# Optimization experiments

Measured on AMD Instinct MI355X. Metric: run time of the kernel, lower is better.

The kernel has to match this reference:

```python
import jax, jax.numpy as jnp
import numpy as np

B, L, H, E = 2, 2048, 16, 64
S, D = L, E


def setup_inputs() -> dict:
    key = jax.random.key(0)
    kq, kk, kv = jax.random.split(key, 3)
    queries = jax.random.normal(kq, (B, L, H, E), dtype=jnp.float32)
    keys = jax.random.normal(kk, (B, S, H, E), dtype=jnp.float32)
    values = jax.random.normal(kv, (B, S, H, D), dtype=jnp.float32)
    return {"queries": queries, "keys": keys, "values": values}


def reference(queries, keys, values):
    # FullAttention forward: mask_flag=True, attn_mask=None -> causal mask,
    # scale=None -> 1/sqrt(E), dropout in eval mode (identity).
    Bq, Lq, Hq, Eq = queries.shape
    Sq = values.shape[1]
    scale = 1.0 / jnp.sqrt(jnp.asarray(Eq, dtype=queries.dtype))
    # [B,H,L,S] score matrix, same as torch.einsum('blhe,bshe->bhls', q, k)
    scores = jnp.einsum('blhe,bshe->bhls', queries, keys)
    # TriangularCausalMask: triu(ones, diagonal=1) -> True above diagonal = masked
    causal = jnp.triu(jnp.ones((Lq, Sq), dtype=bool), k=1)
    scores = jnp.where(causal[None, None, :, :], -jnp.inf, scores)
    A = jax.nn.softmax(scale * scores, axis=-1)
    V = jnp.einsum('bhls,bshd->blhd', A, values)
    return V
```

## Files before the change

### kernel.cpp

```cpp
#include <hip/hip_runtime.h>
#include <hip/hip_bf16.h>


#define B_DIM 2
#define L_DIM 2048
#define H_DIM 16
#define E_DIM 64
#define NEG_INF (-1e30f)
#define CAP   16.0f

typedef __attribute__((ext_vector_type(8))) short short8;
typedef __attribute__((ext_vector_type(4))) float ffrag;

static __device__ __forceinline__ short f2bf(float x) {
    __hip_bfloat16 h = __float2bfloat16(x);
    return *reinterpret_cast<short*>(&h);
}
static __device__ __forceinline__ unsigned pk2(float lo, float hi) {
    __hip_bfloat162 h = __float22bfloat162_rn(make_float2(lo, hi));
    return *reinterpret_cast<unsigned*>(&h);
}

__global__ __launch_bounds__(256, 4)
void attn_fused(const float* __restrict__ Q, const float* __restrict__ K,
                const float* __restrict__ V, float* __restrict__ O) {
    const int lid = blockIdx.x;
    const int x   = lid & 7;
    const int c   = (lid >> 3) & 31;
    const int k4  = lid >> 8;
    const int bh  = x * 4 + k4;
    const int b   = bh >> 4;
    const int h   = bh & 15;
    int strip;
    switch (k4) {
        case 0:  strip = c;              break;
        case 1:  strip = 31 - c;         break;
        case 2:  strip = c ^ 16;         break;
        default: strip = 31 - (c ^ 16);  break;
    }
    const int q0 = strip * 64;

    const int tid  = threadIdx.x;
    const int wave = tid >> 6;
    const int lane = tid & 63;
    const int n16  = lane & 15;
    const int quad = lane >> 4;

    __shared__ short Kt[4096];
    __shared__ short Vt[4096];
    __shared__ short Pq[4096];

    const float sc = 0.125f * 1.44269504088896340736f;
    const int gq = q0 + wave * 16 + n16;

    short8 qf[2];
    {
        const float4* pq = (const float4*)(Q + (((size_t)b * L_DIM + gq) * H_DIM + h) * E_DIM);
#pragma unroll
        for (int kt = 0; kt < 2; ++kt) {
            float4 x0 = pq[kt * 8 + quad * 2];
            float4 x1 = pq[kt * 8 + quad * 2 + 1];
            short8 f;
            f[0] = f2bf(x0.x * sc); f[1] = f2bf(x0.y * sc);
            f[2] = f2bf(x0.z * sc); f[3] = f2bf(x0.w * sc);
            f[4] = f2bf(x1.x * sc); f[5] = f2bf(x1.y * sc);
            f[6] = f2bf(x1.z * sc); f[7] = f2bf(x1.w * sc);
            qf[kt] = f;
        }
    }

    const int rr  = tid >> 2;
    const int c2  = tid & 3;
    const int kOff0 = rr * 64 + (((2 * c2)     ^ (rr & 7)) * 8);
    const int kOff1 = rr * 64 + (((2 * c2 + 1) ^ (rr & 7)) * 8);
    const int kp2 = (tid & 31) * 2;
    const int c8  = (tid >> 5) * 8;

    float4 kr[4], va[2], vb2[2];

    auto load_tile = [&](int kt0) {
        const float4* kg = (const float4*)(K + (((size_t)b * L_DIM + kt0 + rr) * H_DIM + h) * E_DIM + c2 * 16);
        kr[0] = kg[0]; kr[1] = kg[1]; kr[2] = kg[2]; kr[3] = kg[3];
        const float* vp = V + (((size_t)b * L_DIM + kt0 + kp2) * H_DIM + h) * E_DIM + c8;
        const float4* vga = (const float4*)vp;
        const float4* vgb = (const float4*)(vp + H_DIM * E_DIM);
        va[0]  = vga[0]; va[1]  = vga[1];
        vb2[0] = vgb[0]; vb2[1] = vgb[1];
    };
    auto store_tile = [&]() {
        short8 w0, w1;
        w0[0] = f2bf(kr[0].x); w0[1] = f2bf(kr[0].y); w0[2] = f2bf(kr[0].z); w0[3] = f2bf(kr[0].w);
        w0[4] = f2bf(kr[1].x); w0[5] = f2bf(kr[1].y); w0[6] = f2bf(kr[1].z); w0[7] = f2bf(kr[1].w);
        w1[0] = f2bf(kr[2].x); w1[1] = f2bf(kr[2].y); w1[2] = f2bf(kr[2].z); w1[3] = f2bf(kr[2].w);
        w1[4] = f2bf(kr[3].x); w1[5] = f2bf(kr[3].y); w1[6] = f2bf(kr[3].z); w1[7] = f2bf(kr[3].w);
        *(short8*)&Kt[kOff0] = w0;
        *(short8*)&Kt[kOff1] = w1;
        const float* a0 = (const float*)va;
        const float* b0 = (const float*)vb2;
#pragma unroll
        for (int i = 0; i < 8; ++i)
            *(unsigned*)&Vt[(c8 + i) * 64 + (((kp2 >> 3) ^ i) * 8) + (kp2 & 7)] = pk2(a0[i], b0[i]);
    };

    ffrag Oa[4];
#pragma unroll
    for (int nt = 0; nt < 4; ++nt) Oa[nt] = ffrag{0.f, 0.f, 0.f, 0.f};
    float l = 0.f;

    const int sw  = n16 & 7;
    const int fo0 = (quad ^ sw) * 8;
    const int fo1 = fo0 ^ 32;
    short* pbase = &Pq[wave * 1024 + n16 * 64];

    load_tile(0);

    for (int kt0 = 0; kt0 <= q0; kt0 += 64) {
        __syncthreads();
        store_tile();
        __syncthreads();
        if (kt0 + 64 <= q0) load_tile(kt0 + 64);

        ffrag S[4];
#pragma unroll
        for (int mt = 0; mt < 4; ++mt) {
            const int rb = (mt * 16 + n16) * 64;
            short8 a0 = *(const short8*)&Kt[rb + fo0];
            short8 a1 = *(const short8*)&Kt[rb + fo1];
            ffrag z = ffrag{0.f, 0.f, 0.f, 0.f};
            z = __builtin_amdgcn_mfma_f32_16x16x32_bf16(a0, qf[0], z, 0, 0, 0);
            S[mt] = __builtin_amdgcn_mfma_f32_16x16x32_bf16(a1, qf[1], z, 0, 0, 0);
        }

        const bool domask = (kt0 == q0);
        float ps = 0.f;
#pragma unroll
        for (int mt = 0; mt < 4; ++mt) {
            float pv[4];
#pragma unroll
            for (int r = 0; r < 4; ++r) {
                float sv = S[mt][r];
                if (domask && (mt * 16 + quad * 4 + r > wave * 16 + n16)) sv = NEG_INF;
                pv[r] = exp2f(sv - CAP);
                ps += pv[r];
            }
            uint2 w;
            w.x = pk2(pv[0], pv[1]);
            w.y = pk2(pv[2], pv[3]);
            *(uint2*)&pbase[(((2 * mt + (quad >> 1)) ^ sw) * 8) + (quad & 1) * 4] = w;
        }
        ps += __shfl_xor(ps, 16);
        ps += __shfl_xor(ps, 32);
        l += ps;

        short8 pa0 = *(const short8*)&pbase[fo0];
        short8 pa1 = *(const short8*)&pbase[fo1];

#pragma unroll
        for (int nt = 0; nt < 4; ++nt) {
            const int rb = (nt * 16 + n16) * 64;
            short8 b0 = *(const short8*)&Vt[rb + fo0];
            short8 b1 = *(const short8*)&Vt[rb + fo1];
            Oa[nt] = __builtin_amdgcn_mfma_f32_16x16x32_bf16(pa0, b0, Oa[nt], 0, 0, 0);
            Oa[nt] = __builtin_amdgcn_mfma_f32_16x16x32_bf16(pa1, b1, Oa[nt], 0, 0, 0);
        }
    }

#pragma unroll
    for (int r = 0; r < 4; ++r) {
        float li  = __shfl(l, quad * 4 + r);
        float inv = 1.0f / li;
        const int row = q0 + wave * 16 + quad * 4 + r;
        float* op = O + (((size_t)b * L_DIM + row) * H_DIM + h) * E_DIM;
#pragma unroll
        for (int nt = 0; nt < 4; ++nt) op[nt * 16 + n16] = Oa[nt][r] * inv;
    }
}

extern "C" void kernel_launch(void* const* d_in, const int* in_sizes, int n_in,
                              void* d_out, int out_size, void* d_ws, size_t ws_size,
                              hipStream_t stream) {
    const float* Q = (const float*)d_in[0];
    const float* K = (const float*)d_in[1];
    const float* V = (const float*)d_in[2];
    float* O = (float*)d_out;
    attn_fused<<<dim3(1024), 256, 0, stream>>>(Q, K, V, O);
}
```

Baseline: 139.4 us.

## Split KV tiles across two wave groups per block and merge partial outputs

Result: slower. 285.1 us (+104.6%).

```diff
diff --git a/kernel.cpp b/kernel.cpp
--- a/kernel.cpp
+++ b/kernel.cpp
@@ -21,7 +21,7 @@
     return *reinterpret_cast<unsigned*>(&h);
 }
 
-__global__ __launch_bounds__(256, 4)
+__global__ __launch_bounds__(512, 6)
 void attn_fused(const float* __restrict__ Q, const float* __restrict__ K,
                 const float* __restrict__ V, float* __restrict__ O) {
     const int lid = blockIdx.x;
@@ -38,20 +38,25 @@
         case 2:  strip = c ^ 16;         break;
         default: strip = 31 - (c ^ 16);  break;
     }
-    const int q0 = strip * 64;
-
-    const int tid  = threadIdx.x;
-    const int wave = tid >> 6;
-    const int lane = tid & 63;
-    const int n16  = lane & 15;
-    const int quad = lane >> 4;
-
-    __shared__ short Kt[4096];
-    __shared__ short Vt[4096];
-    __shared__ short Pq[4096];
+    const int q0     = strip * 64;
+    const int ntiles = strip + 1;
+    const int T      = (ntiles + 1) >> 1;
+
+    const int tid   = threadIdx.x;
+    const int wave  = tid >> 6;
+    const int grp   = tid >> 8;
+    const int qwave = wave & 3;
+    const int lane  = tid & 63;
+    const int n16   = lane & 15;
+    const int quad  = lane >> 4;
+
+    __shared__ alignas(16) short KV[4][4096];
+    __shared__ alignas(16) short Pq[8192];
+    short* Kt = KV[grp * 2 + 0];
+    short* Vt = KV[grp * 2 + 1];
 
     const float sc = 0.125f * 1.44269504088896340736f;
-    const int gq = q0 + wave * 16 + n16;
+    const int gq = q0 + qwave * 16 + n16;
 
     short8 qf[2];
     {
@@ -69,12 +74,13 @@
         }
     }
 
-    const int rr  = tid >> 2;
-    const int c2  = tid & 3;
+    const int gtid = tid & 255;
+    const int rr  = gtid >> 2;
+    const int c2  = gtid & 3;
     const int kOff0 = rr * 64 + (((2 * c2)     ^ (rr & 7)) * 8);
     const int kOff1 = rr * 64 + (((2 * c2 + 1) ^ (rr & 7)) * 8);
-    const int kp2 = (tid & 31) * 2;
-    const int c8  = (tid >> 5) * 8;
+    const int kp2 = (gtid & 31) * 2;
+    const int c8  = ((gtid >> 5) & 7) * 8;
 
     float4 kr[4], va[2], vb2[2];
 
@@ -112,67 +118,92 @@
     const int fo1 = fo0 ^ 32;
     short* pbase = &Pq[wave * 1024 + n16 * 64];
 
-    load_tile(0);
-
-    for (int kt0 = 0; kt0 <= q0; kt0 += 64) {
+    if (grp == 0 || ntiles > 1) load_tile(grp << 6);
+
+    for (int t = 0; t < T; ++t) {
+        const int it    = 2 * t + grp;
+        const bool valid = (it < ntiles);
         __syncthreads();
-        store_tile();
+        if (valid) store_tile();
         __syncthreads();
-        if (kt0 + 64 <= q0) load_tile(kt0 + 64);
-
-        ffrag S[4];
-#pragma unroll
-        for (int mt = 0; mt < 4; ++mt) {
-            const int rb = (mt * 16 + n16) * 64;
-            short8 a0 = *(const short8*)&Kt[rb + fo0];
-            short8 a1 = *(const short8*)&Kt[rb + fo1];
-            ffrag z = ffrag{0.f, 0.f, 0.f, 0.f};
-            z = __builtin_amdgcn_mfma_f32_16x16x32_bf16(a0, qf[0], z, 0, 0, 0);
-            S[mt] = __builtin_amdgcn_mfma_f32_16x16x32_bf16(a1, qf[1], z, 0, 0, 0);
+        if (it + 2 < ntiles) load_tile((it + 2) << 6);
+
+        if (valid) {
+            ffrag S[4];
+            __builtin_amdgcn_s_setprio(1);
+#pragma unroll
+            for (int mt = 0; mt < 4; ++mt) {
+                const int rb = (mt * 16 + n16) * 64;
+                short8 a0 = *(const short8*)&Kt[rb + fo0];
+                short8 a1 = *(const short8*)&Kt[rb + fo1];
+                ffrag z = ffrag{0.f, 0.f, 0.f, 0.f};
+                z = __builtin_amdgcn_mfma_f32_16x16x32_bf16(a0, qf[0], z, 0, 0, 0);
+                S[mt] = __builtin_amdgcn_mfma_f32_16x16x32_bf16(a1, qf[1], z, 0, 0, 0);
+            }
+            __builtin_amdgcn_s_setprio(0);
+
+            const bool domask = (it == ntiles - 1);
+            float ps = 0.f;
+#pragma unroll
+            for (int mt = 0; mt < 4; ++mt) {
+                float pv[4];
+#pragma unroll
+                for (int r = 0; r < 4; ++r) {
+                    float sv = S[mt][r];
+                    if (domask && (mt * 16 + quad * 4 + r > qwave * 16 + n16)) sv = NEG_INF;
+                    pv[r] = exp2f(sv - CAP);
+                    ps += pv[r];
+                }
+                uint2 w;
+                w.x = pk2(pv[0], pv[1]);
+                w.y = pk2(pv[2], pv[3]);
+                *(uint2*)&pbase[(((2 * mt + (quad >> 1)) ^ sw) * 8) + (quad & 1) * 4] = w;
+            }
+            ps += __shfl_xor(ps, 16);
+            ps += __shfl_xor(ps, 32);
+            l += ps;
+
+            short8 pa0 = *(const short8*)&pbase[fo0];
+            short8 pa1 = *(const short8*)&pbase[fo1];
+
+            __builtin_amdgcn_s_setprio(1);
+#pragma unroll
+            for (int nt = 0; nt < 4; ++nt) {
+                const int rb = (nt * 16 + n16) * 64;
+                short8 b0 = *(const short8*)&Vt[rb + fo0];
+                short8 b1 = *(const short8*)&Vt[rb + fo1];
+                Oa[nt] = __builtin_amdgcn_mfma_f32_16x16x32_bf16(pa0, b0, Oa[nt], 0, 0, 0);
+                Oa[nt] = __builtin_amdgcn_mfma_f32_16x16x32_bf16(pa1, b1, Oa[nt], 0, 0, 0);
+            }
+            __builtin_amdgcn_s_setprio(0);
         }
-
-        const bool domask = (kt0 == q0);
-        float ps = 0.f;
-#pragma unroll
-        for (int mt = 0; mt < 4; ++mt) {
-            float pv[4];
-#pragma unroll
-            for (int r = 0; r < 4; ++r) {
-                float sv = S[mt][r];
-                if (domask && (mt * 16 + quad * 4 + r > wave * 16 + n16)) sv = NEG_INF;
-                pv[r] = exp2f(sv - CAP);
-                ps += pv[r];
-            }
-            uint2 w;
-            w.x = pk2(pv[0], pv[1]);
-            w.y = pk2(pv[2], pv[3]);
-            *(uint2*)&pbase[(((2 * mt + (quad >> 1)) ^ sw) * 8) + (quad & 1) * 4] = w;
+    }
+
+    __syncthreads();
+    float* fO = (float*)&KV[0][0];
+    float* fL = (float*)&KV[2][0];
+    if (grp == 1) {
+        ffrag* dst = (ffrag*)(fO + ((qwave * 64 + lane) << 4));
+#pragma unroll
+        for (int nt = 0; nt < 4; ++nt) dst[nt] = Oa[nt];
+        fL[qwave * 64 + lane] = l;
+    }
+    __syncthreads();
+    if (grp == 0) {
+        const ffrag* src = (const ffrag*)(fO + ((qwave * 64 + lane) << 4));
+#pragma unroll
+        for (int nt = 0; nt < 4; ++nt) Oa[nt] += src[nt];
+        l += fL[qwave * 64 + lane];
+
+#pragma unroll
+        for (int r = 0; r < 4; ++r) {
+            float li  = __shfl(l, quad * 4 + r);
+            float inv = 1.0f / li;
+            const int row = q0 + qwave * 16 + quad * 4 + r;
+            float* op = O + (((size_t)b * L_DIM + row) * H_DIM + h) * E_DIM;
+#pragma unroll
+            for (int nt = 0; nt < 4; ++nt) op[nt * 16 + n16] = Oa[nt][r] * inv;
         }
-        ps += __shfl_xor(ps, 16);
-        ps += __shfl_xor(ps, 32);
-        l += ps;
-
-        short8 pa0 = *(const short8*)&pbase[fo0];
-        short8 pa1 = *(const short8*)&pbase[fo1];
-
-#pragma unroll
-        for (int nt = 0; nt < 4; ++nt) {
-            const int rb = (nt * 16 + n16) * 64;
-            short8 b0 = *(const short8*)&Vt[rb + fo0];
-            short8 b1 = *(const short8*)&Vt[rb + fo1];
-            Oa[nt] = __builtin_amdgcn_mfma_f32_16x16x32_bf16(pa0, b0, Oa[nt], 0, 0, 0);
-            Oa[nt] = __builtin_amdgcn_mfma_f32_16x16x32_bf16(pa1, b1, Oa[nt], 0, 0, 0);
-        }
-    }
-
-#pragma unroll
-    for (int r = 0; r < 4; ++r) {
-        float li  = __shfl(l, quad * 4 + r);
-        float inv = 1.0f / li;
-        const int row = q0 + wave * 16 + quad * 4 + r;
-        float* op = O + (((size_t)b * L_DIM + row) * H_DIM + h) * E_DIM;
-#pragma unroll
-        for (int nt = 0; nt < 4; ++nt) op[nt * 16 + n16] = Oa[nt][r] * inv;
     }
 }
 
@@ -183,5 +214,5 @@
     const float* K = (const float*)d_in[1];
     const float* V = (const float*)d_in[2];
     float* O = (float*)d_out;
-    attn_fused<<<dim3(1024), 256, 0, stream>>>(Q, K, V, O);
-}
+    attn_fused<<<dim3(1024), 512, 0, stream>>>(Q, K, V, O);
+}
```
